# Kernel optimization log

Hardware: AMD Instinct MI355X
Metric: run time of the kernel (lower is better)

The kernel has to match this reference:

```python
import jax, jax.numpy as jnp
import numpy as np

MARGIN = 1.0
B, D_FEAT = 4096, 256


def setup_inputs() -> dict:
    key = jax.random.key(0)
    return {"inputs": jax.random.normal(key, (B, D_FEAT), dtype=jnp.float32)}


def reference(inputs):
    bsz = inputs.shape[0]
    P = bsz // 2  # number of positive pairs
    # pairwise similarity, scaled as in the original (/128.0)
    D = jnp.matmul(inputs, inputs.T) / 128.0          # [B, B]
    Dexpm = jnp.exp(MARGIN + D)                        # [B, B]

    # Row 2p over odd columns (2k+1), row 2p+1 over even columns (2l)
    Rodd = Dexpm[0::2, 1::2]                           # [P, P]: Dexpm[2p, 2k+1]
    Reven = Dexpm[1::2, 0::2]                          # [P, P]: Dexpm[2p+1, 2l]

    p = jnp.arange(P)
    k = jnp.arange(P)
    # Faithful to the original code's exclusion bug: k != pos_j (=2p+1), l != pos_i (=2p)
    mask_i = (k[None, :] != (2 * p + 1)[:, None]).astype(Dexpm.dtype)  # [P, P]
    mask_j = (k[None, :] != (2 * p)[:, None]).astype(Dexpm.dtype)      # [P, P]

    neg_ik = jnp.sum(Rodd * mask_i, axis=1)            # [P]
    neg_jl = jnp.sum(Reven * mask_j, axis=1)           # [P]

    Dpos = D[2 * p, 2 * p + 1]                         # [P] positive-pair similarity
    J = jnp.log(1e-8 + neg_ik + neg_jl) - Dpos         # [P]
    return jnp.sum(jnp.maximum(J, 0.0) ** 2) / bsz
```

## Files before the change

### kernel.cpp

```cpp
#include <hip/hip_runtime.h>

#define PN 2048

typedef __attribute__((ext_vector_type(8))) short short8;
typedef __attribute__((ext_vector_type(4))) float f32x4;

static __device__ __forceinline__ unsigned int pk_bf2(float lo, float hi) {
    unsigned int ul = __float_as_uint(lo);
    unsigned int uh = __float_as_uint(hi);
    ul = (ul + 0x7fffu + ((ul >> 16) & 1u)) >> 16;
    uh = (uh + 0x7fffu + ((uh >> 16) & 1u)) >> 16;
    return ul | (uh << 16);
}


__global__ __launch_bounds__(512, 2) void sml_mfma(
    const float* __restrict__ X, float* __restrict__ Srow, float* __restrict__ Scol,
    float* __restrict__ Dpos, float* __restrict__ out)
{
    __shared__ __align__(16) unsigned int A_s[2 * 128 * 64];
    __shared__ __align__(16) unsigned int B_s[2 * 128 * 64];
    __shared__ float red[4][128];

    const int bx = blockIdx.x, by = blockIdx.y;
    const int t = threadIdx.x;
    const int lane = t & 63, wid = t >> 6;
    const int wr = wid >> 2, wc = wid & 3;
    const int g4 = lane >> 4, rl = lane & 15;

    if (bx == 0 && by == 0 && t == 0) out[0] = 0.f;

    const int s  = t & 15;
    const int r0 = t >> 4;

    const float* aP[4];
    const float* bP[4];
    #pragma unroll
    for (int q = 0; q < 4; ++q) {
        const int r = r0 + 32 * q;
        aP[q] = X + (size_t)(2 * (bx * 128 + r)) * 256 + s * 8;
        bP[q] = X + (size_t)(2 * (by * 128 + r) + 1) * 256 + s * 8;
    }

    f32x4 acc[4][2];
    #pragma unroll
    for (int i = 0; i < 4; ++i)
        #pragma unroll
        for (int j = 0; j < 2; ++j) acc[i][j] = (f32x4){0.f, 0.f, 0.f, 0.f};

    float4 a0[4][2], b0[4][2];
    #pragma unroll
    for (int q = 0; q < 4; ++q) {
        a0[q][0] = *(const float4*)(aP[q]);     a0[q][1] = *(const float4*)(aP[q] + 4);
        b0[q][0] = *(const float4*)(bP[q]);     b0[q][1] = *(const float4*)(bP[q] + 4);
    }
    #pragma unroll
    for (int q = 0; q < 4; ++q) {
        const int r  = r0 + 32 * q;
        const int sw = (s ^ (r & 15)) << 2;
        uint4 wa = { pk_bf2(a0[q][0].x, a0[q][0].y), pk_bf2(a0[q][0].z, a0[q][0].w),
                     pk_bf2(a0[q][1].x, a0[q][1].y), pk_bf2(a0[q][1].z, a0[q][1].w) };
        uint4 wb = { pk_bf2(b0[q][0].x, b0[q][0].y), pk_bf2(b0[q][0].z, b0[q][0].w),
                     pk_bf2(b0[q][1].x, b0[q][1].y), pk_bf2(b0[q][1].z, b0[q][1].w) };
        *(uint4*)&A_s[r * 64 + sw] = wa;
        *(uint4*)&B_s[r * 64 + sw] = wb;
    }
    __syncthreads();

    float4 a1[4][2], b1[4][2];
    #pragma unroll
    for (int q = 0; q < 4; ++q) {
        a1[q][0] = *(const float4*)(aP[q] + 128); a1[q][1] = *(const float4*)(aP[q] + 132);
        b1[q][0] = *(const float4*)(bP[q] + 128); b1[q][1] = *(const float4*)(bP[q] + 132);
    }

    #pragma unroll
    for (int kk = 0; kk < 4; ++kk) {
        short8 af[4], bfj[2];
        #pragma unroll
        for (int i = 0; i < 4; ++i) {
            const int r  = wr * 64 + i * 16 + rl;
            const int sl = ((kk << 2) + g4) ^ (r & 15);
            af[i] = *(const short8*)&A_s[r * 64 + sl * 4];
        }
        #pragma unroll
        for (int j = 0; j < 2; ++j) {
            const int r  = wc * 32 + j * 16 + rl;
            const int sl = ((kk << 2) + g4) ^ (r & 15);
            bfj[j] = *(const short8*)&B_s[r * 64 + sl * 4];
        }
        #pragma unroll
        for (int i = 0; i < 4; ++i)
            #pragma unroll
            for (int j = 0; j < 2; ++j)
                acc[i][j] = __builtin_amdgcn_mfma_f32_16x16x32_bf16(af[i], bfj[j], acc[i][j], 0, 0, 0);
    }

    #pragma unroll
    for (int q = 0; q < 4; ++q) {
        const int r  = r0 + 32 * q;
        const int sw = (s ^ (r & 15)) << 2;
        uint4 wa = { pk_bf2(a1[q][0].x, a1[q][0].y), pk_bf2(a1[q][0].z, a1[q][0].w),
                     pk_bf2(a1[q][1].x, a1[q][1].y), pk_bf2(a1[q][1].z, a1[q][1].w) };
        uint4 wb = { pk_bf2(b1[q][0].x, b1[q][0].y), pk_bf2(b1[q][0].z, b1[q][0].w),
                     pk_bf2(b1[q][1].x, b1[q][1].y), pk_bf2(b1[q][1].z, b1[q][1].w) };
        *(uint4*)&A_s[8192 + r * 64 + sw] = wa;
        *(uint4*)&B_s[8192 + r * 64 + sw] = wb;
    }
    __syncthreads();

    #pragma unroll
    for (int kk = 0; kk < 4; ++kk) {
        short8 af[4], bfj[2];
        #pragma unroll
        for (int i = 0; i < 4; ++i) {
            const int r  = wr * 64 + i * 16 + rl;
            const int sl = ((kk << 2) + g4) ^ (r & 15);
            af[i] = *(const short8*)&A_s[8192 + r * 64 + sl * 4];
        }
        #pragma unroll
        for (int j = 0; j < 2; ++j) {
            const int r  = wc * 32 + j * 16 + rl;
            const int sl = ((kk << 2) + g4) ^ (r & 15);
            bfj[j] = *(const short8*)&B_s[8192 + r * 64 + sl * 4];
        }
        #pragma unroll
        for (int i = 0; i < 4; ++i)
            #pragma unroll
            for (int j = 0; j < 2; ++j)
                acc[i][j] = __builtin_amdgcn_mfma_f32_16x16x32_bf16(af[i], bfj[j], acc[i][j], 0, 0, 0);
    }

    float rs[4][4];
    float cs[2] = {0.f, 0.f};
    #pragma unroll
    for (int i = 0; i < 4; ++i)
        #pragma unroll
        for (int rg = 0; rg < 4; ++rg) rs[i][rg] = 0.f;

    #pragma unroll
    for (int i = 0; i < 4; ++i) {
        #pragma unroll
        for (int j = 0; j < 2; ++j) {
            const int kg = by * 128 + wc * 32 + j * 16 + rl;
            #pragma unroll
            for (int rg = 0; rg < 4; ++rg) {
                const int pg = bx * 128 + wr * 64 + i * 16 + g4 * 4 + rg;
                const float c = acc[i][j][rg] * (1.f / 128.f);
                const float e = __expf(1.f + c);
                if (kg == pg) Dpos[pg] = c;
                rs[i][rg] += (kg == 2 * pg + 1) ? 0.f : e;
                cs[j]     += (pg == 2 * kg)     ? 0.f : e;
            }
        }
    }

    #pragma unroll
    for (int i = 0; i < 4; ++i) {
        #pragma unroll
        for (int rg = 0; rg < 4; ++rg) {
            float v = rs[i][rg];
            v += __shfl_xor(v, 1); v += __shfl_xor(v, 2);
            v += __shfl_xor(v, 4); v += __shfl_xor(v, 8);
            if (rl == 0) red[wc][wr * 64 + i * 16 + g4 * 4 + rg] = v;
        }
    }
    __syncthreads();
    if (t < 128)
        Srow[by * PN + bx * 128 + t] = red[0][t] + red[1][t] + red[2][t] + red[3][t];
    __syncthreads();

    #pragma unroll
    for (int j = 0; j < 2; ++j) {
        float v = cs[j];
        v += __shfl_xor(v, 16); v += __shfl_xor(v, 32);
        if (g4 == 0) red[wr][wc * 32 + j * 16 + rl] = v;
    }
    __syncthreads();
    if (t < 128)
        Scol[bx * PN + by * 128 + t] = red[0][t] + red[1][t];
}

__global__ __launch_bounds__(64) void sml_finish(
    const float* __restrict__ Srow, const float* __restrict__ Scol,
    const float* __restrict__ Dpos, float* __restrict__ out)
{
    const int t = threadIdx.x;
    const int p = blockIdx.x * 64 + t;
    float ssum = 0.f;
    #pragma unroll
    for (int g = 0; g < 16; ++g) ssum += Srow[g * PN + p];
    #pragma unroll
    for (int g = 0; g < 16; ++g) ssum += Scol[g * PN + p];
    const float J = __logf(1e-8f + ssum) - Dpos[p];
    const float v = fmaxf(J, 0.f);
    float local = v * v;
    #pragma unroll
    for (int m = 1; m < 64; m <<= 1) local += __shfl_xor(local, m);
    if (t == 0) atomicAdd(out, local * (1.f / 4096.f));
}

extern "C" void kernel_launch(void* const* d_in, const int* in_sizes, int n_in,
                              void* d_out, int out_size, void* d_ws, size_t ws_size,
                              hipStream_t stream) {
    const float* X = (const float*)d_in[0];
    float* ws   = (float*)d_ws;
    float* Srow = ws;
    float* Scol = Srow + 16 * PN;
    float* Dpos = Scol + 16 * PN;
    float* out  = (float*)d_out;

    sml_mfma<<<dim3(16, 16), dim3(512), 0, stream>>>(X, Srow, Scol, Dpos, out);
    sml_finish<<<32, dim3(64), 0, stream>>>(Srow, Scol, Dpos, out);
}
```

Baseline: 16.37 us.

## Load full K slab at once and write per-wave partial sums directly to global

```diff
diff --git a/kernel.cpp b/kernel.cpp
--- a/kernel.cpp
+++ b/kernel.cpp
@@ -18,9 +18,8 @@
     const float* __restrict__ X, float* __restrict__ Srow, float* __restrict__ Scol,
     float* __restrict__ Dpos, float* __restrict__ out)
 {
-    __shared__ __align__(16) unsigned int A_s[2 * 128 * 64];
-    __shared__ __align__(16) unsigned int B_s[2 * 128 * 64];
-    __shared__ float red[4][128];
+    __shared__ __align__(16) unsigned int A_s[128 * 128];
+    __shared__ __align__(16) unsigned int B_s[128 * 128];
 
     const int bx = blockIdx.x, by = blockIdx.y;
     const int t = threadIdx.x;
@@ -30,17 +29,48 @@
 
     if (bx == 0 && by == 0 && t == 0) out[0] = 0.f;
 
-    const int s  = t & 15;
-    const int r0 = t >> 4;
+    const int s  = t & 31;
+    const int r0 = t >> 5;
 
-    const float* aP[4];
-    const float* bP[4];
+    const float* aP[8];
+    const float* bP[8];
     #pragma unroll
-    for (int q = 0; q < 4; ++q) {
-        const int r = r0 + 32 * q;
+    for (int q = 0; q < 8; ++q) {
+        const int r = r0 + 16 * q;
         aP[q] = X + (size_t)(2 * (bx * 128 + r)) * 256 + s * 8;
         bP[q] = X + (size_t)(2 * (by * 128 + r) + 1) * 256 + s * 8;
     }
+
+    float4 aV[8][2], bV[8][2];
+    #pragma unroll
+    for (int q = 0; q < 8; ++q) {
+        aV[q][0] = *(const float4*)(aP[q]);
+        aV[q][1] = *(const float4*)(aP[q] + 4);
+    }
+    #pragma unroll
+    for (int q = 0; q < 8; ++q) {
+        bV[q][0] = *(const float4*)(bP[q]);
+        bV[q][1] = *(const float4*)(bP[q] + 4);
+    }
+
+    #pragma unroll
+    for (int q = 0; q < 8; ++q) {
+        const int r  = r0 + 16 * q;
+        const int sw = (s ^ (r & 31)) << 2;
+        uint4 wa = { pk_bf2(aV[q][0].x, aV[q][0].y), pk_bf2(aV[q][0].z, aV[q][0].w),
+                     pk_bf2(aV[q][1].x, aV[q][1].y), pk_bf2(aV[q][1].z, aV[q][1].w) };
+        *(uint4*)&A_s[r * 128 + sw] = wa;
+    }
+    #pragma unroll
+    for (int q = 0; q < 8; ++q) {
+        const int r  = r0 + 16 * q;
+        const int sw = (s ^ (r & 31)) << 2;
+        uint4 wb = { pk_bf2(bV[q][0].x, bV[q][0].y), pk_bf2(bV[q][0].z, bV[q][0].w),
+                     pk_bf2(bV[q][1].x, bV[q][1].y), pk_bf2(bV[q][1].z, bV[q][1].w) };
+        *(uint4*)&B_s[r * 128 + sw] = wb;
+    }
+
+    __syncthreads();
 
     f32x4 acc[4][2];
     #pragma unroll
@@ -48,81 +78,21 @@
         #pragma unroll
         for (int j = 0; j < 2; ++j) acc[i][j] = (f32x4){0.f, 0.f, 0.f, 0.f};
 
-    float4 a0[4][2], b0[4][2];
     #pragma unroll
-    for (int q = 0; q < 4; ++q) {
-        a0[q][0] = *(const float4*)(aP[q]);     a0[q][1] = *(const float4*)(aP[q] + 4);
-        b0[q][0] = *(const float4*)(bP[q]);     b0[q][1] = *(const float4*)(bP[q] + 4);
-    }
-    #pragma unroll
-    for (int q = 0; q < 4; ++q) {
-        const int r  = r0 + 32 * q;
-        const int sw = (s ^ (r & 15)) << 2;
-        uint4 wa = { pk_bf2(a0[q][0].x, a0[q][0].y), pk_bf2(a0[q][0].z, a0[q][0].w),
-                     pk_bf2(a0[q][1].x, a0[q][1].y), pk_bf2(a0[q][1].z, a0[q][1].w) };
-        uint4 wb = { pk_bf2(b0[q][0].x, b0[q][0].y), pk_bf2(b0[q][0].z, b0[q][0].w),
-                     pk_bf2(b0[q][1].x, b0[q][1].y), pk_bf2(b0[q][1].z, b0[q][1].w) };
-        *(uint4*)&A_s[r * 64 + sw] = wa;
-        *(uint4*)&B_s[r * 64 + sw] = wb;
-    }
-    __syncthreads();
-
-    float4 a1[4][2], b1[4][2];
-    #pragma unroll
-    for (int q = 0; q < 4; ++q) {
-        a1[q][0] = *(const float4*)(aP[q] + 128); a1[q][1] = *(const float4*)(aP[q] + 132);
-        b1[q][0] = *(const float4*)(bP[q] + 128); b1[q][1] = *(const float4*)(bP[q] + 132);
-    }
-
-    #pragma unroll
-    for (int kk = 0; kk < 4; ++kk) {
+    for (int step = 0; step < 8; ++step) {
+        const int c = (step << 2) + g4;
         short8 af[4], bfj[2];
         #pragma unroll
         for (int i = 0; i < 4; ++i) {
             const int r  = wr * 64 + i * 16 + rl;
-            const int sl = ((kk << 2) + g4) ^ (r & 15);
-            af[i] = *(const short8*)&A_s[r * 64 + sl * 4];
+            const int sl = c ^ (r & 31);
+            af[i] = *(const short8*)&A_s[r * 128 + sl * 4];
         }
         #pragma unroll
         for (int j = 0; j < 2; ++j) {
             const int r  = wc * 32 + j * 16 + rl;
-            const int sl = ((kk << 2) + g4) ^ (r & 15);
-            bfj[j] = *(const short8*)&B_s[r * 64 + sl * 4];
-        }
-        #pragma unroll
-        for (int i = 0; i < 4; ++i)
-            #pragma unroll
-            for (int j = 0; j < 2; ++j)
-                acc[i][j] = __builtin_amdgcn_mfma_f32_16x16x32_bf16(af[i], bfj[j], acc[i][j], 0, 0, 0);
-    }
-
-    #pragma unroll
-    for (int q = 0; q < 4; ++q) {
-        const int r  = r0 + 32 * q;
-        const int sw = (s ^ (r & 15)) << 2;
-        uint4 wa = { pk_bf2(a1[q][0].x, a1[q][0].y), pk_bf2(a1[q][0].z, a1[q][0].w),
-                     pk_bf2(a1[q][1].x, a1[q][1].y), pk_bf2(a1[q][1].z, a1[q][1].w) };
-        uint4 wb = { pk_bf2(b1[q][0].x, b1[q][0].y), pk_bf2(b1[q][0].z, b1[q][0].w),
-                     pk_bf2(b1[q][1].x, b1[q][1].y), pk_bf2(b1[q][1].z, b1[q][1].w) };
-        *(uint4*)&A_s[8192 + r * 64 + sw] = wa;
-        *(uint4*)&B_s[8192 + r * 64 + sw] = wb;
-    }
-    __syncthreads();
-
-    #pragma unroll
-    for (int kk = 0; kk < 4; ++kk) {
-        short8 af[4], bfj[2];
-        #pragma unroll
-        for (int i = 0; i < 4; ++i) {
-            const int r  = wr * 64 + i * 16 + rl;
-            const int sl = ((kk << 2) + g4) ^ (r & 15);
-            af[i] = *(const short8*)&A_s[8192 + r * 64 + sl * 4];
-        }
-        #pragma unroll
-        for (int j = 0; j < 2; ++j) {
-            const int r  = wc * 32 + j * 16 + rl;
-            const int sl = ((kk << 2) + g4) ^ (r & 15);
-            bfj[j] = *(const short8*)&B_s[8192 + r * 64 + sl * 4];
+            const int sl = c ^ (r & 31);
+            bfj[j] = *(const short8*)&B_s[r * 128 + sl * 4];
         }
         #pragma unroll
         for (int i = 0; i < 4; ++i)
@@ -155,6 +125,7 @@
         }
     }
 
+    float* SrowS = Srow + (size_t)(by * 4 + wc) * PN;
     #pragma unroll
     for (int i = 0; i < 4; ++i) {
         #pragma unroll
@@ -162,23 +133,18 @@
             float v = rs[i][rg];
             v += __shfl_xor(v, 1); v += __shfl_xor(v, 2);
             v += __shfl_xor(v, 4); v += __shfl_xor(v, 8);
-            if (rl == 0) red[wc][wr * 64 + i * 16 + g4 * 4 + rg] = v;
+            if (rl == 0)
+                SrowS[bx * 128 + wr * 64 + i * 16 + g4 * 4 + rg] = v;
         }
     }
-    __syncthreads();
-    if (t < 128)
-        Srow[by * PN + bx * 128 + t] = red[0][t] + red[1][t] + red[2][t] + red[3][t];
-    __syncthreads();
-
+    float* ScolS = Scol + (size_t)(bx * 2 + wr) * PN;
     #pragma unroll
     for (int j = 0; j < 2; ++j) {
         float v = cs[j];
         v += __shfl_xor(v, 16); v += __shfl_xor(v, 32);
-        if (g4 == 0) red[wr][wc * 32 + j * 16 + rl] = v;
+        if (g4 == 0)
+            ScolS[by * 128 + wc * 32 + j * 16 + rl] = v;
     }
-    __syncthreads();
-    if (t < 128)
-        Scol[bx * PN + by * 128 + t] = red[0][t] + red[1][t];
 }
 
 __global__ __launch_bounds__(64) void sml_finish(
@@ -189,9 +155,9 @@
     const int p = blockIdx.x * 64 + t;
     float ssum = 0.f;
     #pragma unroll
-    for (int g = 0; g < 16; ++g) ssum += Srow[g * PN + p];
+    for (int g = 0; g < 64; ++g) ssum += Srow[g * PN + p];
     #pragma unroll
-    for (int g = 0; g < 16; ++g) ssum += Scol[g * PN + p];
+    for (int g = 0; g < 32; ++g) ssum += Scol[g * PN + p];
     const float J = __logf(1e-8f + ssum) - Dpos[p];
     const float v = fmaxf(J, 0.f);
     float local = v * v;
@@ -206,8 +172,8 @@
     const float* X = (const float*)d_in[0];
     float* ws   = (float*)d_ws;
     float* Srow = ws;
-    float* Scol = Srow + 16 * PN;
-    float* Dpos = Scol + 16 * PN;
+    float* Scol = Srow + 64 * PN;
+    float* Dpos = Scol + 32 * PN;
     float* out  = (float*)d_out;
 
     sml_mfma<<<dim3(16, 16), dim3(512), 0, stream>>>(X, Srow, Scol, Dpos, out);
```

Result: slower. 18.93 us (+15.6%).
